# Performance work log

Hardware: AMD Instinct MI355X
Metric: run time of the kernel (lower is better)

The kernel has to match this reference:

```python
import jax, jax.numpy as jnp
import numpy as np

B, C, H, W = 4, 256, 64, 64
EPS = 1e-5

def conv1x1(x, w, b):
    # x: [B,Cin,H,W], w: [Cout,Cin], b: [Cout]
    return jnp.einsum('bchw,oc->bohw', x, w) + b[None, :, None, None]

def setup_inputs() -> dict:
    key = jax.random.key(0)
    ks = jax.random.split(key, 16)
    s = 1.0 / np.sqrt(C)
    d = {
        'x1': jax.random.normal(ks[0], (B, C, H, W), jnp.float32),
        'x2': jax.random.normal(ks[1], (B, C, H, W), jnp.float32),
        'q_w': jax.random.normal(ks[2], (C, C), jnp.float32) * s,
        'q_b': jnp.zeros((C,), jnp.float32),
        'k_w': jax.random.normal(ks[3], (C, C), jnp.float32) * s,
        'k_b': jnp.zeros((C,), jnp.float32),
        'v_w': jax.random.normal(ks[4], (C, C), jnp.float32) * s,
        'v_b': jnp.zeros((C,), jnp.float32),
        'proj_w': jax.random.normal(ks[5], (C, C), jnp.float32) * s,
        'proj_b': jnp.zeros((C,), jnp.float32),
        'bn_gamma': jnp.ones((C,), jnp.float32),
        'bn_beta': jnp.zeros((C,), jnp.float32),
        'bn_mean': jax.random.normal(ks[6], (C,), jnp.float32) * 0.1,
        'bn_var': jax.random.uniform(ks[7], (C,), jnp.float32, 0.5, 1.5),
        'gate_w': jax.random.normal(ks[8], (1, 2 * C), jnp.float32) * (1.0 / np.sqrt(2 * C)),
        'gate_b': jnp.zeros((1,), jnp.float32),
    }
    return d

def reference(x1, x2, q_w, q_b, k_w, k_b, v_w, v_b, proj_w, proj_b,
              bn_gamma, bn_beta, bn_mean, bn_var, gate_w, gate_b):
    b, c, h, w = x1.shape
    n = h * w
    scale = c ** (-0.5)
    q = conv1x1(x1, q_w, q_b).reshape(b, c, n)   # [B,C,N]
    k = conv1x1(x2, k_w, k_b).reshape(b, c, n)
    v = conv1x1(x2, v_w, v_b).reshape(b, c, n)
    attn = jnp.einsum('bcn,bcm->bnm', q, k) * scale      # [B,N,N]
    attn = jax.nn.softmax(attn, axis=-1)
    fusion = jnp.einsum('bcm,bnm->bcn', v, attn)          # v @ attn^T
    fusion = fusion.reshape(b, c, h, w)
    # proj: conv1x1 -> BN (eval, running stats) -> ReLU
    fusion = conv1x1(fusion, proj_w, proj_b)
    fusion = (fusion - bn_mean[None, :, None, None]) * (
        bn_gamma[None, :, None, None] * jax.lax.rsqrt(bn_var + EPS)[None, :, None, None]
    ) + bn_beta[None, :, None, None]
    fusion = jax.nn.relu(fusion)
    gate = jax.nn.sigmoid(conv1x1(jnp.concatenate([x1, x2], axis=1), gate_w, gate_b))  # [B,1,H,W]
    return x1 + gate * fusion
```

## Files before the change

kernel.cpp:

```cpp
#include <hip/hip_runtime.h>
#include <hip/hip_bf16.h>

#define NB   4
#define C    256
#define NPIX 4096
#define EPSV 1e-5f
#define K2   0.09016844f
#define KVB  32
#define NSPLIT 4
#define NKVS (NPIX / NSPLIT)
#define NSTEPS (NKVS / KVB)

typedef __bf16 bf16x8 __attribute__((ext_vector_type(8)));
typedef float  f32x4  __attribute__((ext_vector_type(4)));
typedef float  f32x16 __attribute__((ext_vector_type(16)));
typedef unsigned int u32x4 __attribute__((ext_vector_type(4)));
typedef __hip_bfloat16 bf16;

__device__ __forceinline__ void gload16(const void* g, void* l) {
    __builtin_amdgcn_global_load_lds(
        (const __attribute__((address_space(1))) void*)g,
        (__attribute__((address_space(3))) void*)l, 16, 0, 0);
}

__global__ __launch_bounds__(256) void k_wcvt(
    const float* __restrict__ qw, const float* __restrict__ kw,
    const float* __restrict__ vw, const float* __restrict__ pw,
    bf16* __restrict__ wb)
{
    const int i = blockIdx.x * 256 + threadIdx.x;
    const int p = i >> 16, rem = i & 65535;
    const int o = rem >> 8, cp = rem & 255;
    const int c = cp ^ ((o & 7) << 3);
    const float* w = (p == 0) ? qw : (p == 1) ? kw : (p == 2) ? vw : pw;
    wb[i] = __float2bfloat16(w[o * 256 + c]);
}

__global__ __launch_bounds__(256) void k_transpose(
    const float* __restrict__ x1, const float* __restrict__ x2,
    const float* __restrict__ gate_w,
    bf16* __restrict__ xt1, bf16* __restrict__ xt2, float* __restrict__ gate_ws)
{
    __shared__ float tile[64][65];
    const int nt = blockIdx.x, ct = blockIdx.y, z = blockIdx.z;
    const int b = z >> 1, which = z & 1;
    const float* x = which ? x2 : x1;
    bf16* xt = which ? xt2 : xt1;
    const int t = threadIdx.x;
    const int n0 = nt * 64, c0 = ct * 64;

    const float* xp = x + ((size_t)b * C + c0) * NPIX + n0;
#pragma unroll
    for (int i = 0; i < 16; ++i) {
        int cl = (t >> 6) + i * 4, nl = t & 63;
        tile[cl][nl] = xp[(size_t)cl * NPIX + nl];
    }
    __syncthreads();

    {
        int nl = t & 63, qq = t >> 6;
        float s = 0.f;
#pragma unroll
        for (int i = 0; i < 16; ++i) {
            int cl = qq * 16 + i;
            s += tile[cl][nl] * gate_w[which * C + c0 + cl];
        }
        atomicAdd(&gate_ws[b * NPIX + n0 + nl], s);
    }

    bf16* xtp = xt + ((size_t)b * NPIX + n0) * C + c0;
#pragma unroll
    for (int i = 0; i < 16; ++i) {
        int nl = (t >> 6) + i * 4, cl = t & 63;
        xtp[(size_t)nl * C + cl] = __float2bfloat16(tile[cl][nl]);
    }
}

__global__ __launch_bounds__(256) void k_qkv(
    const bf16* __restrict__ xt1, const bf16* __restrict__ xt2,
    const bf16* __restrict__ wb,
    const float* __restrict__ qb, const float* __restrict__ kb,
    const float* __restrict__ vb,
    bf16* __restrict__ Qt, bf16* __restrict__ Kt, bf16* __restrict__ Vv)
{
    __shared__ __align__(16) char wl[32768];
    const int nblk = blockIdx.x, ot = blockIdx.y, zp = blockIdx.z;
    const int b = zp / 3, pidx = zp % 3;
    const bf16* xt = (pidx == 0) ? xt1 : xt2;
    const float* bias = (pidx == 0) ? qb : (pidx == 1) ? kb : vb;
    const int o0 = ot * 64;
    const int t = threadIdx.x;
    const int wave = t >> 6, lane = t & 63;
    const int g = lane >> 4, l15 = lane & 15;

    {
        const char* src = (const char*)(wb + ((size_t)pidx * C + o0) * C);
#pragma unroll
        for (int i = 0; i < 8; ++i) {
            const int L = i * 4096 + t * 16;
            gload16(src + L, wl + L);
        }
    }
    asm volatile("s_waitcnt vmcnt(0)" ::: "memory");
    __syncthreads();

    bf16x8 a[4][8];
#pragma unroll
    for (int ns = 0; ns < 4; ++ns) {
        const bf16* xrow = xt + ((size_t)b * NPIX + nblk * 256 + wave * 64 + ns * 16 + l15) * C;
#pragma unroll
        for (int cb = 0; cb < 8; ++cb)
            a[ns][cb] = *reinterpret_cast<const bf16x8*>(xrow + cb * 32 + 8 * g);
    }

#pragma unroll
    for (int os = 0; os < 4; ++os) {
        const int oo = o0 + os * 16;
        bf16x8 wf[8];
#pragma unroll
        for (int cb = 0; cb < 8; ++cb)
            wf[cb] = *reinterpret_cast<const bf16x8*>(
                wl + (os * 16 + l15) * 512 + ((cb * 64 + 16 * g) ^ ((l15 & 7) << 4)));

        f32x4 acc[4] = {{0,0,0,0},{0,0,0,0},{0,0,0,0},{0,0,0,0}};
#pragma unroll
        for (int cb = 0; cb < 8; ++cb) {
#pragma unroll
            for (int ns = 0; ns < 4; ++ns) {
                if (pidx < 2)
                    acc[ns] = __builtin_amdgcn_mfma_f32_16x16x32_bf16(a[ns][cb], wf[cb], acc[ns], 0, 0, 0);
                else
                    acc[ns] = __builtin_amdgcn_mfma_f32_16x16x32_bf16(wf[cb], a[ns][cb], acc[ns], 0, 0, 0);
            }
        }

        if (pidx < 2) {
            const float bv = bias[oo + l15];
            bf16* Qk = (pidx == 0) ? Qt : Kt;
#pragma unroll
            for (int ns = 0; ns < 4; ++ns) {
                const int n0 = nblk * 256 + wave * 64 + ns * 16;
                bf16* dst = Qk + ((size_t)b * NPIX + n0 + 4 * g) * C + oo + l15;
#pragma unroll
                for (int r = 0; r < 4; ++r)
                    dst[(size_t)r * C] = __float2bfloat16(acc[ns][r] + bv);
            }
        } else {
#pragma unroll
            for (int ns = 0; ns < 4; ++ns) {
                const int n0 = nblk * 256 + wave * 64 + ns * 16;
                bf16* dst = Vv + ((size_t)b * C + oo + 4 * g) * NPIX + n0 + l15;
#pragma unroll
                for (int r = 0; r < 4; ++r)
                    dst[(size_t)r * NPIX] = __float2bfloat16(acc[ns][r] + bias[oo + 4 * g + r]);
            }
        }
    }
}

#define SMEM_ATTN 65536
#define SZP ((size_t)NPIX * C)

__global__ __launch_bounds__(256, 2) void k_attn(
    const bf16* __restrict__ Qt, const bf16* __restrict__ Kt,
    const bf16* __restrict__ Vv, bf16* __restrict__ O0,
    bf16* __restrict__ O1, float2* __restrict__ mlws)
{
    extern __shared__ __align__(16) char smem[];
    const int id = blockIdx.x;
    const int combo = id & 15, nt = id >> 4;
    const int b = combo >> 2, split = combo & 3;
    const int m_base = split * NKVS;
    const int tid = threadIdx.x;
    const int wave = tid >> 6, lane = tid & 63;
    const int dl = lane & 31, hi = lane >> 5;
    const int n0 = nt * 128 + wave * 32;

    const bf16* Kg = Kt + (size_t)b * NPIX * C;
    const bf16* Vg = Vv + (size_t)b * C * NPIX;

    int o_k[4], o_v[4];
#pragma unroll
    for (int p = 0; p < 4; ++p) {
        const int L = p * 4096 + tid * 16;
        const int kv = L >> 9, colx = L & 511;
        const int col = colx ^ ((kv & 7) << 4);
        o_k[p] = kv * C + (col >> 1);
        const int R = L >> 7, colx2 = L & 127;
        const int col2 = colx2 ^ (((L >> 8) & 7) << 4);
        const int d = 2 * R + (col2 >> 6);
        o_v[p] = d * NPIX + ((col2 & 63) >> 1);
    }

    bf16x8 q[16];
    const bf16* qrow = Qt + ((size_t)b * NPIX + n0 + dl) * C + 8 * hi;
#pragma unroll
    for (int cs = 0; cs < 16; ++cs)
        q[cs] = *reinterpret_cast<const bf16x8*>(qrow + cs * 16);

    const int kRow = dl * 512, kmask = (lane & 7) << 4;
    const int vRow = (dl >> 1) * 128;
    const int vc0  = (((dl & 1) << 6) | (16 * hi)) ^ (((dl >> 2) & 7) << 4);

    f32x16 o[8];
#pragma unroll
    for (int i = 0; i < 8; ++i)
#pragma unroll
        for (int j = 0; j < 16; ++j) o[i][j] = 0.f;
    float m_run = -3.0e38f, l_run = 0.f;

    auto stage = [&](int buf, int m0) {
        char* kd = smem + buf * 16384;
        char* vd = smem + 32768 + buf * 16384;
#pragma unroll
        for (int p = 0; p < 4; ++p) {
            gload16(Kg + (size_t)m0 * C + o_k[p], kd + p * 4096 + tid * 16);
            gload16(Vg + o_v[p] + m0,            vd + p * 4096 + tid * 16);
        }
    };

    stage(0, m_base);
    asm volatile("s_waitcnt vmcnt(0)" ::: "memory");
    __syncthreads();

    for (int t = 0; t < NSTEPS; ++t) {
        const int buf = t & 1;
        if (t + 1 < NSTEPS) stage(buf ^ 1, m_base + (t + 1) * KVB);

        const char* Kl = smem + buf * 16384;
        const char* Vl = smem + 32768 + buf * 16384;

        f32x16 s;
#pragma unroll
        for (int j = 0; j < 16; ++j) s[j] = 0.f;
        __builtin_amdgcn_s_setprio(1);
#pragma unroll
        for (int cs = 0; cs < 16; ++cs) {
            bf16x8 kf = *reinterpret_cast<const bf16x8*>(
                Kl + kRow + ((cs * 32 + 16 * hi) ^ kmask));
            s = __builtin_amdgcn_mfma_f32_32x32x16_bf16(kf, q[cs], s, 0, 0, 0);
        }
        __builtin_amdgcn_s_setprio(0);

#pragma unroll
        for (int j = 0; j < 16; ++j) s[j] = s[j] * K2;
        float mx = s[0];
#pragma unroll
        for (int j = 1; j < 16; ++j) mx = fmaxf(mx, s[j]);
        mx = fmaxf(mx, __shfl_xor(mx, 32));

        if (!__all(mx <= m_run + 8.f)) {
            const float mnew = fmaxf(m_run, mx);
            const float cf = exp2f(m_run - mnew);
            m_run = mnew;
            l_run *= cf;
#pragma unroll
            for (int i = 0; i < 8; ++i)
#pragma unroll
                for (int j = 0; j < 16; ++j) o[i][j] *= cf;
        }

        float psum = 0.f;
#pragma unroll
        for (int j = 0; j < 16; ++j) {
            s[j] = exp2f(s[j] - m_run);
            psum += s[j];
        }
        psum += __shfl_xor(psum, 32);
        l_run += psum;

        unsigned w[8];
#pragma unroll
        for (int i = 0; i < 8; ++i) {
            asm("v_cvt_pk_bf16_f32 %0, %1, %2"
                : "=v"(w[i]) : "v"(s[2 * i]), "v"(s[2 * i + 1]));
        }
        asm("v_permlane32_swap_b32 %0, %1" : "+v"(w[0]), "+v"(w[2]));
        asm("v_permlane32_swap_b32 %0, %1" : "+v"(w[1]), "+v"(w[3]));
        asm("v_permlane32_swap_b32 %0, %1" : "+v"(w[4]), "+v"(w[6]));
        asm("v_permlane32_swap_b32 %0, %1" : "+v"(w[5]), "+v"(w[7]));
        const bf16x8 pb0 = __builtin_bit_cast(bf16x8, (u32x4){w[0], w[1], w[2], w[3]});
        const bf16x8 pb1 = __builtin_bit_cast(bf16x8, (u32x4){w[4], w[5], w[6], w[7]});

        __builtin_amdgcn_s_setprio(1);
#pragma unroll
        for (int dt = 0; dt < 8; ++dt) {
            bf16x8 vf0 = *reinterpret_cast<const bf16x8*>(Vl + dt * 2048 + vRow + vc0);
            o[dt] = __builtin_amdgcn_mfma_f32_32x32x16_bf16(vf0, pb0, o[dt], 0, 0, 0);
            bf16x8 vf1 = *reinterpret_cast<const bf16x8*>(Vl + dt * 2048 + vRow + (vc0 ^ 32));
            o[dt] = __builtin_amdgcn_mfma_f32_32x32x16_bf16(vf1, pb1, o[dt], 0, 0, 0);
        }
        __builtin_amdgcn_s_setprio(0);

        asm volatile("s_waitcnt vmcnt(0)" ::: "memory");
        __syncthreads();
    }

    const int pp = split * NB + b;
    bf16* base = (pp < 8) ? (O0 + (size_t)pp * SZP) : (O1 + (size_t)(pp - 8) * SZP);
    const float invl = 1.0f / l_run;
    bf16* orow = base + (size_t)(n0 + dl) * C;
#pragma unroll
    for (int dt = 0; dt < 8; ++dt) {
#pragma unroll
        for (int a = 0; a < 4; ++a) {
            bf16 t4[4];
#pragma unroll
            for (int r = 0; r < 4; ++r)
                t4[r] = __float2bfloat16(o[dt][4 * a + r] * invl);
            *reinterpret_cast<uint64_t*>(orow + dt * 32 + 8 * a + 4 * hi) =
                *reinterpret_cast<uint64_t*>(t4);
        }
    }
    if (lane < 32)
        mlws[(size_t)pp * NPIX + n0 + dl] = make_float2(m_run, l_run);
}

__global__ __launch_bounds__(256) void k_combine(
    const bf16* __restrict__ O0, const bf16* __restrict__ O1,
    const float2* __restrict__ ml, bf16* __restrict__ Ot)
{
    const int tid = blockIdx.x * 256 + threadIdx.x;
    const int c8 = tid & 31;
    const int rest = tid >> 5;
    const int n = rest & 4095;
    const int b = rest >> 12;

    float2 a[NSPLIT];
#pragma unroll
    for (int s = 0; s < NSPLIT; ++s)
        a[s] = ml[(size_t)(s * NB + b) * NPIX + n];
    float M = fmaxf(fmaxf(a[0].x, a[1].x), fmaxf(a[2].x, a[3].x));
    float w[NSPLIT], tot = 0.f;
#pragma unroll
    for (int s = 0; s < NSPLIT; ++s) { w[s] = exp2f(a[s].x - M) * a[s].y; tot += w[s]; }
    float rs = 1.0f / tot;
#pragma unroll
    for (int s = 0; s < NSPLIT; ++s) w[s] *= rs;

    const size_t off = (size_t)n * C + c8 * 8;
    float acc[8] = {0,0,0,0,0,0,0,0};
#pragma unroll
    for (int s = 0; s < NSPLIT; ++s) {
        const int pp = s * NB + b;
        const bf16* src = ((pp < 8) ? (O0 + (size_t)pp * SZP)
                                    : (O1 + (size_t)(pp - 8) * SZP)) + off;
        bf16x8 x = *reinterpret_cast<const bf16x8*>(src);
#pragma unroll
        for (int j = 0; j < 8; ++j) acc[j] += w[s] * (float)x[j];
    }
    bf16 outv[8];
#pragma unroll
    for (int j = 0; j < 8; ++j) outv[j] = __float2bfloat16(acc[j]);
    *reinterpret_cast<bf16x8*>(Ot + ((size_t)b * NPIX + n) * C + c8 * 8) =
        *reinterpret_cast<bf16x8*>(outv);
}

__global__ __launch_bounds__(256) void k_proj(
    const bf16* __restrict__ Ot, const bf16* __restrict__ wb,
    const float* __restrict__ pb, const float* __restrict__ bn_g,
    const float* __restrict__ bn_b, const float* __restrict__ bn_m,
    const float* __restrict__ bn_v, const float* __restrict__ gate_ws,
    const float* __restrict__ gate_b, const float* __restrict__ x1,
    float* __restrict__ out)
{
    __shared__ __align__(16) char wl[32768];
    const int nblk = blockIdx.x, ot = blockIdx.y, b = blockIdx.z;
    const int o0 = ot * 64;
    const int t = threadIdx.x;
    const int wave = t >> 6, lane = t & 63;
    const int g = lane >> 4, l15 = lane & 15;

    {
        const char* src = (const char*)(wb + ((size_t)3 * C + o0) * C);
#pragma unroll
        for (int i = 0; i < 8; ++i) {
            const int L = i * 4096 + t * 16;
            gload16(src + L, wl + L);
        }
    }
    asm volatile("s_waitcnt vmcnt(0)" ::: "memory");
    __syncthreads();

    bf16x8 bfr[2][8];
#pragma unroll
    for (int ns = 0; ns < 2; ++ns) {
        const bf16* orow = Ot + ((size_t)b * NPIX + nblk * 128 + wave * 32 + ns * 16 + l15) * C;
#pragma unroll
        for (int cb = 0; cb < 8; ++cb)
            bfr[ns][cb] = *reinterpret_cast<const bf16x8*>(orow + cb * 32 + 8 * g);
    }
    const float gb = gate_b[0];

#pragma unroll
    for (int os = 0; os < 4; ++os) {
        const int oo = o0 + os * 16;
        bf16x8 wf[8];
#pragma unroll
        for (int cb = 0; cb < 8; ++cb)
            wf[cb] = *reinterpret_cast<const bf16x8*>(
                wl + (os * 16 + l15) * 512 + ((cb * 64 + 16 * g) ^ ((l15 & 7) << 4)));

        f32x4 acc[2] = {{0,0,0,0},{0,0,0,0}};
#pragma unroll
        for (int cb = 0; cb < 8; ++cb) {
            acc[0] = __builtin_amdgcn_mfma_f32_16x16x32_bf16(wf[cb], bfr[0][cb], acc[0], 0, 0, 0);
            acc[1] = __builtin_amdgcn_mfma_f32_16x16x32_bf16(wf[cb], bfr[1][cb], acc[1], 0, 0, 0);
        }

#pragma unroll
        for (int ns = 0; ns < 2; ++ns) {
            const int n0 = nblk * 128 + wave * 32 + ns * 16;
            float gsum = gate_ws[b * NPIX + n0 + l15];
            float gate = 1.f / (1.f + __expf(-(gsum + gb)));
#pragma unroll
            for (int r = 0; r < 4; ++r) {
                int oc = oo + 4 * g + r;
                float scl = bn_g[oc] * rsqrtf(bn_v[oc] + EPSV);
                float v = (acc[ns][r] + pb[oc] - bn_m[oc]) * scl + bn_b[oc];
                v = fmaxf(v, 0.f);
                size_t idx = ((size_t)b * C + oc) * NPIX + n0 + l15;
                out[idx] = x1[idx] + gate * v;
            }
        }
    }
}

extern "C" void kernel_launch(void* const* d_in, const int* in_sizes, int n_in,
                              void* d_out, int out_size, void* d_ws, size_t ws_size,
                              hipStream_t stream)
{
    const float* x1  = (const float*)d_in[0];
    const float* x2  = (const float*)d_in[1];
    const float* q_w = (const float*)d_in[2];
    const float* q_b = (const float*)d_in[3];
    const float* k_w = (const float*)d_in[4];
    const float* k_b = (const float*)d_in[5];
    const float* v_w = (const float*)d_in[6];
    const float* v_b = (const float*)d_in[7];
    const float* p_w = (const float*)d_in[8];
    const float* p_b = (const float*)d_in[9];
    const float* bn_g = (const float*)d_in[10];
    const float* bn_b = (const float*)d_in[11];
    const float* bn_m = (const float*)d_in[12];
    const float* bn_v = (const float*)d_in[13];
    const float* g_w  = (const float*)d_in[14];
    const float* g_b  = (const float*)d_in[15];
    float* out = (float*)d_out;

    const size_t szBF = (size_t)NB * NPIX * C * sizeof(bf16);
    char* p = (char*)d_ws;
    bf16* xt1 = (bf16*)p; p += szBF;
    bf16* xt2 = (bf16*)p; p += szBF;
    bf16* Qt  = (bf16*)p; p += szBF;
    bf16* Kt  = (bf16*)p; p += szBF;
    bf16* Vv  = (bf16*)p; p += szBF;
    float* gate_ws = (float*)p; p += (size_t)NB * NPIX * sizeof(float);
    float2* mlws = (float2*)p; p += (size_t)16 * NPIX * sizeof(float2);
    bf16* wb = (bf16*)p;

    bf16* O0 = (bf16*)d_out;
    bf16* O1 = xt1;
    bf16* Ot = Qt;

    hipFuncSetAttribute((const void*)k_attn,
                        hipFuncAttributeMaxDynamicSharedMemorySize, SMEM_ATTN);

    hipMemsetAsync(gate_ws, 0, (size_t)NB * NPIX * sizeof(float), stream);
    k_wcvt    <<<dim3(1024), 256, 0, stream>>>(q_w, k_w, v_w, p_w, wb);
    k_transpose<<<dim3(64, 4, 8),  256, 0, stream>>>(x1, x2, g_w, xt1, xt2, gate_ws);
    k_qkv     <<<dim3(16, 4, 12), 256, 0, stream>>>(xt1, xt2, wb, q_b, k_b, v_b,
                                                    Qt, Kt, Vv);
    k_attn    <<<dim3(512), 256, SMEM_ATTN, stream>>>(Qt, Kt, Vv, O0, O1, mlws);
    k_combine <<<dim3(2048), 256, 0, stream>>>(O0, O1, mlws, Ot);
    k_proj    <<<dim3(32, 4, 4),  256, 0, stream>>>(Ot, wb, p_b, bn_g, bn_b, bn_m,
                                                    bn_v, gate_ws, g_b, x1, out);
}
```

Before: 163.2 us.

## Fold softmax scale into Q, seed fixed running max, merge weight conversion launch

Pre-scales Q by the softmax constant in the projection kernel, so the attention loop skips per-score multiplies. The running max now starts at a fixed value, so the rescale branch and its cross-lane shuffle rarely execute. The weight bf16 conversion is merged into the transpose kernel as an extra grid slice, removing one launch. A fixed initial max risks underflow only if scores are much smaller than the seed, and bf16 rounding of the scaled Q differs slightly.

```diff
diff --git a/kernel.cpp b/kernel.cpp
--- a/kernel.cpp
+++ b/kernel.cpp
@@ -6,6 +6,7 @@
 #define NPIX 4096
 #define EPSV 1e-5f
 #define K2   0.09016844f
+#define MFIX 24.0f
 #define KVB  32
 #define NSPLIT 4
 #define NKVS (NPIX / NSPLIT)
@@ -23,30 +24,39 @@
         (__attribute__((address_space(3))) void*)l, 16, 0, 0);
 }
 
-__global__ __launch_bounds__(256) void k_wcvt(
-    const float* __restrict__ qw, const float* __restrict__ kw,
-    const float* __restrict__ vw, const float* __restrict__ pw,
-    bf16* __restrict__ wb)
-{
-    const int i = blockIdx.x * 256 + threadIdx.x;
-    const int p = i >> 16, rem = i & 65535;
-    const int o = rem >> 8, cp = rem & 255;
-    const int c = cp ^ ((o & 7) << 3);
-    const float* w = (p == 0) ? qw : (p == 1) ? kw : (p == 2) ? vw : pw;
-    wb[i] = __float2bfloat16(w[o * 256 + c]);
-}
-
 __global__ __launch_bounds__(256) void k_transpose(
     const float* __restrict__ x1, const float* __restrict__ x2,
     const float* __restrict__ gate_w,
-    bf16* __restrict__ xt1, bf16* __restrict__ xt2, float* __restrict__ gate_ws)
+    const float* __restrict__ qw, const float* __restrict__ kw,
+    const float* __restrict__ vw, const float* __restrict__ pw,
+    bf16* __restrict__ xt1, bf16* __restrict__ xt2,
+    float* __restrict__ gate_ws, bf16* __restrict__ wb)
 {
     __shared__ float tile[64][65];
-    const int nt = blockIdx.x, ct = blockIdx.y, z = blockIdx.z;
+    const int t = threadIdx.x;
+    const int z = blockIdx.z;
+
+    if (z == 8) {
+        const int sub = blockIdx.x * 4 + blockIdx.y;
+        const int i0 = sub * 1024 + t * 4;
+        bf16 t4[4];
+#pragma unroll
+        for (int j = 0; j < 4; ++j) {
+            const int i = i0 + j;
+            const int p = i >> 16, rem = i & 65535;
+            const int o = rem >> 8, cp = rem & 255;
+            const int c = cp ^ ((o & 7) << 3);
+            const float* w = (p == 0) ? qw : (p == 1) ? kw : (p == 2) ? vw : pw;
+            t4[j] = __float2bfloat16(w[o * 256 + c]);
+        }
+        *reinterpret_cast<uint64_t*>(wb + i0) = *reinterpret_cast<uint64_t*>(t4);
+        return;
+    }
+
+    const int nt = blockIdx.x, ct = blockIdx.y;
     const int b = z >> 1, which = z & 1;
     const float* x = which ? x2 : x1;
     bf16* xt = which ? xt2 : xt1;
-    const int t = threadIdx.x;
     const int n0 = nt * 64, c0 = ct * 64;
 
     const float* xp = x + ((size_t)b * C + c0) * NPIX + n0;
@@ -136,6 +146,7 @@
 
         if (pidx < 2) {
             const float bv = bias[oo + l15];
+            const float scl = (pidx == 0) ? K2 : 1.0f;
             bf16* Qk = (pidx == 0) ? Qt : Kt;
 #pragma unroll
             for (int ns = 0; ns < 4; ++ns) {
@@ -143,7 +154,7 @@
                 bf16* dst = Qk + ((size_t)b * NPIX + n0 + 4 * g) * C + oo + l15;
 #pragma unroll
                 for (int r = 0; r < 4; ++r)
-                    dst[(size_t)r * C] = __float2bfloat16(acc[ns][r] + bv);
+                    dst[(size_t)r * C] = __float2bfloat16((acc[ns][r] + bv) * scl);
             }
         } else {
 #pragma unroll
@@ -207,7 +218,7 @@
     for (int i = 0; i < 8; ++i)
 #pragma unroll
         for (int j = 0; j < 16; ++j) o[i][j] = 0.f;
-    float m_run = -3.0e38f, l_run = 0.f;
+    float m_run = MFIX, l_run = 0.f;
 
     auto stage = [&](int buf, int m0) {
         char* kd = smem + buf * 16384;
@@ -242,16 +253,16 @@
         }
         __builtin_amdgcn_s_setprio(0);
 
-#pragma unroll
-        for (int j = 0; j < 16; ++j) s[j] = s[j] * K2;
-        float mx = s[0];
-#pragma unroll
-        for (int j = 1; j < 16; ++j) mx = fmaxf(mx, s[j]);
-        mx = fmaxf(mx, __shfl_xor(mx, 32));
-
-        if (!__all(mx <= m_run + 8.f)) {
-            const float mnew = fmaxf(m_run, mx);
-            const float cf = exp2f(m_run - mnew);
+        float m0v = fmaxf(s[0], s[1]),  m1v = fmaxf(s[2], s[3]);
+        float m2v = fmaxf(s[4], s[5]),  m3v = fmaxf(s[6], s[7]);
+        float m4v = fmaxf(s[8], s[9]),  m5v = fmaxf(s[10], s[11]);
+        float m6v = fmaxf(s[12], s[13]), m7v = fmaxf(s[14], s[15]);
+        float mx = fmaxf(fmaxf(fmaxf(m0v, m1v), fmaxf(m2v, m3v)),
+                         fmaxf(fmaxf(m4v, m5v), fmaxf(m6v, m7v)));
+        if (!__all(mx <= m_run)) {
+            float mxr = fmaxf(mx, __shfl_xor(mx, 32));
+            float mnew = fmaxf(m_run, mxr);
+            float cf = exp2f(m_run - mnew);
             m_run = mnew;
             l_run *= cf;
 #pragma unroll
@@ -467,8 +478,8 @@
                         hipFuncAttributeMaxDynamicSharedMemorySize, SMEM_ATTN);
 
     hipMemsetAsync(gate_ws, 0, (size_t)NB * NPIX * sizeof(float), stream);
-    k_wcvt    <<<dim3(1024), 256, 0, stream>>>(q_w, k_w, v_w, p_w, wb);
-    k_transpose<<<dim3(64, 4, 8),  256, 0, stream>>>(x1, x2, g_w, xt1, xt2, gate_ws);
+    k_transpose<<<dim3(64, 4, 9),  256, 0, stream>>>(x1, x2, g_w, q_w, k_w, v_w, p_w,
+                                                     xt1, xt2, gate_ws, wb);
     k_qkv     <<<dim3(16, 4, 12), 256, 0, stream>>>(xt1, xt2, wb, q_b, k_b, v_b,
                                                     Qt, Kt, Vv);
     k_attn    <<<dim3(512), 256, SMEM_ATTN, stream>>>(Qt, Kt, Vv, O0, O1, mlws);
```

New measurement: 157.2 us, median of 2. -3.7%, faster.
